# Kernel optimization log

Hardware: AMD Instinct MI355X
Metric: run time of the kernel (lower is better)

## Reference

```python
import jax, jax.numpy as jnp
import numpy as np

B, C, D, Hh, W = 2, 320, 4, 16, 16
N = D * Hh * W          # 1024 nodes
NH = 8                  # num_heads
DH = C // NH            # 40
L = 2                   # num_layers
A, EPD = 16, 64         # da_prior tokens, encode_prior_dim
EDGE_SCALE = 32 ** -0.5 # GraphEdgeFeature dim_head=32
SCALE = DH ** -0.5
EPS = 1e-5


def _ln(x, g, b):
    m = x.mean(-1, keepdims=True)
    v = ((x - m) ** 2).mean(-1, keepdims=True)
    return (x - m) * jax.lax.rsqrt(v + EPS) * g + b


def setup_inputs() -> dict:
    key = jax.random.key(0)
    ks = jax.random.split(key, 16)
    std = 0.02 / np.sqrt(L)
    inp = {
        'x': jax.random.normal(ks[0], (B, C, D, Hh, W), jnp.float32),
        'da_prior': jax.random.normal(ks[1], (B, A, EPD), jnp.float32),
        # GraphEdgeFeature.to_qk (no bias), init std 0.02/sqrt(24)
        'qk_w': jax.random.normal(ks[2], (2 * C, C), jnp.float32) * (0.02 / np.sqrt(24)),
        # fc_prior
        'fcp_w': jax.random.normal(ks[3], (C, EPD), jnp.float32) * 0.02,
        'fcp_b': jnp.zeros((C,), jnp.float32),
        # per-layer (stacked over L)
        'ln1_g': jnp.ones((L, C), jnp.float32),
        'ln1_b': jnp.zeros((L, C), jnp.float32),
        'gln_g': jnp.ones((L, C), jnp.float32),
        'gln_b': jnp.zeros((L, C), jnp.float32),
        'qkv_w': jax.random.normal(ks[4], (L, 3 * C, C), jnp.float32) * std,
        'qkv_b': jnp.zeros((L, 3 * C), jnp.float32),
        'proj_w': jax.random.normal(ks[5], (L, C, C), jnp.float32) * std,
        'proj_b': jnp.zeros((L, C), jnp.float32),
        # expand Conv2d(1, NH, 1): weight [NH], bias [NH]
        'exp_w': jax.random.normal(ks[6], (L, NH), jnp.float32),
        'exp_b': jnp.zeros((L, NH), jnp.float32),
        # reduce Conv2d(NH, 1, 1): weight [NH], bias scalar
        'red_w': jax.random.normal(ks[7], (L, NH), jnp.float32) / np.sqrt(NH),
        'red_b': jnp.zeros((L,), jnp.float32),
    }
    return inp


def _forward(x, da_prior, qk_w, fcp_w, fcp_b, ln1_g, ln1_b, gln_g, gln_b,
             qkv_w, qkv_b, proj_w, proj_b, exp_w, exp_b, red_w, red_b):
    node = x.reshape(B, C, N)                       # [B,C,N]
    # ---- GraphEdgeFeature: full-dim QK attention over nodes ----
    xt = node.transpose(0, 2, 1)                    # [B,N,C]
    qk = xt @ qk_w.T                                # [B,N,2C]
    q_e, k_e = jnp.split(qk, 2, axis=-1)
    edge = jax.nn.softmax(jnp.einsum('bqc,bkc->bqk', q_e, k_e) * EDGE_SCALE, axis=-1)  # [B,N,N]
    # ---- fc_prior ----
    da = da_prior @ fcp_w.T + fcp_b                 # [B,A,C]
    s = da.sum(axis=1)                              # [B,C] (sum over 'a' in einsum bnc,bca->bnc)
    for l in range(L):
        # block norm1 over channel dim
        nt = _ln(node.transpose(0, 2, 1), ln1_g[l], ln1_b[l])   # [B,N,C]
        # torch.einsum('bnn,bnc->bnc') takes the DIAGONAL of edge
        diag = jnp.diagonal(edge, axis1=1, axis2=2)             # [B,N]
        node2 = diag[:, :, None] * nt * s[:, None, :] + nt      # [B,N,C]
        y = _ln(node2, gln_g[l], gln_b[l])
        qkv = (y @ qkv_w[l].T + qkv_b[l]).reshape(B, N, 3, NH, DH)
        qkv = qkv.transpose(2, 0, 3, 1, 4)                      # [3,B,H,N,DH]
        q, k, v = qkv[0], qkv[1], qkv[2]
        attn = jnp.einsum('bhnd,bhmd->bhnm', q, k) * SCALE
        attn = attn + edge[:, None] * exp_w[l][None, :, None, None] + exp_b[l][None, :, None, None]
        a = jax.nn.softmax(attn, axis=-1)                       # [B,H,N,N]
        node_out = jnp.einsum('bhnm,bhmd->bhnd', a, v).transpose(0, 2, 1, 3).reshape(B, N, C)
        edge_new = jnp.einsum('bhnm,h->bnm', a + attn, red_w[l]) + red_b[l]  # [B,N,N]
        ws = jax.nn.softmax(edge_new, axis=-1)
        wsum = (ws * edge_new).sum(-1)                          # [B,N]
        node_out = node_out + wsum[:, :, None]                  # fc=Identity, broadcast
        node_out = node_out @ proj_w[l].T + proj_b[l]
        node = node_out.transpose(0, 2, 1)                      # [B,C,N]
        edge = edge + edge_new
    return node.reshape(B, C, D, Hh, W)


def reference(x, da_prior, qk_w, fcp_w, fcp_b, ln1_g, ln1_b, gln_g, gln_b,
              qkv_w, qkv_b, proj_w, proj_b, exp_w, exp_b, red_w, red_b):
    return _forward(x, da_prior, qk_w, fcp_w, fcp_b, ln1_g, ln1_b, gln_g, gln_b,
                    qkv_w, qkv_b, proj_w, proj_b, exp_w, exp_b, red_w, red_b)
```

## Files before the change

### kernel.cpp

```cpp
#include <hip/hip_runtime.h>
#include <math.h>

#define EDGE_SCALE 0.17677669529663687f
#define ATT_SCALE  0.15811388300841897f
#define INV_ATT    6.324555320336759f
#define LN_EPS 1e-5f

typedef __attribute__((ext_vector_type(8))) short bf8;
typedef __attribute__((ext_vector_type(4))) float f32x4;

__device__ __forceinline__ f32x4 mfma16(bf8 a, bf8 b, f32x4 c) {
  return __builtin_amdgcn_mfma_f32_16x16x32_bf16(a, b, c, 0, 0, 0);
}
__device__ __forceinline__ unsigned short f2bf(float f) {
  union { float f; unsigned u; } v; v.f = f;
  unsigned r = v.u + 0x7FFF + ((v.u >> 16) & 1);
  return (unsigned short)(r >> 16);
}
__device__ __forceinline__ float bf2f(unsigned short h) {
  union { unsigned u; float f; } v; v.u = ((unsigned)h) << 16;
  return v.f;
}
__device__ __forceinline__ float wave_max(float v) {
  #pragma unroll
  for (int o = 32; o > 0; o >>= 1) v = fmaxf(v, __shfl_xor(v, o));
  return v;
}
__device__ __forceinline__ float wave_sum(float v) {
  #pragma unroll
  for (int o = 32; o > 0; o >>= 1) v += __shfl_xor(v, o);
  return v;
}

__global__ __launch_bounds__(256) void k_trans(const float* __restrict__ x,
    float* __restrict__ node, unsigned short* __restrict__ nodebf) {
  __shared__ float tile[32][33];
  const int b = blockIdx.z;
  const int n0 = blockIdx.x * 32, c0 = blockIdx.y * 32;
  const int tx = threadIdx.x & 31, ty = threadIdx.x >> 5;
  #pragma unroll
  for (int k = 0; k < 4; ++k) {
    int c = c0 + ty + 8 * k;
    tile[ty + 8 * k][tx] = x[((size_t)b * 320 + c) * 1024 + n0 + tx];
  }
  __syncthreads();
  #pragma unroll
  for (int k = 0; k < 4; ++k) {
    int n = n0 + ty + 8 * k;
    float v = tile[tx][ty + 8 * k];
    size_t idx = ((size_t)b * 1024 + n) * 320 + c0 + tx;
    node[idx] = v;
    nodebf[idx] = f2bf(v);
  }
}

__global__ __launch_bounds__(320) void k_svec(const float* __restrict__ da,
    const float* __restrict__ fw, const float* __restrict__ fb, float* __restrict__ sv) {
  __shared__ float ds[64];
  const int b = blockIdx.x, t = threadIdx.x;
  if (t < 64) {
    float a = 0.f;
    #pragma unroll
    for (int i = 0; i < 16; ++i) a += da[b * 1024 + i * 64 + t];
    ds[t] = a;
  }
  __syncthreads();
  if (t < 320) {
    float acc = 16.f * fb[t];
    #pragma unroll
    for (int e = 0; e < 64; ++e) acc = fmaf(ds[e], fw[t * 64 + e], acc);
    sv[b * 320 + t] = acc;
  }
}

__global__ void k_wcvt(const float* __restrict__ a, int na,
                       const float* __restrict__ b, int nb,
                       const float* __restrict__ c, int nc,
                       unsigned short* __restrict__ out) {
  int tot = na + nb + nc;
  for (int i = blockIdx.x * blockDim.x + threadIdx.x; i < tot; i += gridDim.x * blockDim.x) {
    float v = (i < na) ? a[i] : ((i < na + nb) ? b[i - na] : c[i - na - nb]);
    out[i] = f2bf(v);
  }
}

__global__ __launch_bounds__(256, 4) void k_mgemm(
    const unsigned short* __restrict__ A, const unsigned short* __restrict__ W,
    const float* __restrict__ bias, void* p0, void* p1, void* p2, int mode) {
  __shared__ float smem[64 * 65];
  const int t = threadIdx.x, w = t >> 6, lane = t & 63;
  const int q16 = lane >> 4, l16 = lane & 15;
  const int rt = blockIdx.x * 64, jt = blockIdx.y * 64;
  f32x4 acc[4];
  #pragma unroll
  for (int i = 0; i < 4; ++i)
    #pragma unroll
    for (int j = 0; j < 4; ++j) acc[i][j] = 0.f;
  const unsigned short* ap = A + (size_t)(rt + 16 * w + l16) * 320 + q16 * 8;
  const unsigned short* wp = W + (size_t)(jt + l16) * 320 + q16 * 8;
  for (int kc = 0; kc < 10; ++kc) {
    bf8 af = *(const bf8*)(ap + kc * 32);
    #pragma unroll
    for (int ct = 0; ct < 4; ++ct) {
      bf8 bf = *(const bf8*)(wp + (size_t)ct * 16 * 320 + kc * 32);
      acc[ct] = mfma16(af, bf, acc[ct]);
    }
  }
  if (mode == 0 || mode == 1) {
    #pragma unroll
    for (int ct = 0; ct < 4; ++ct) {
      int col = jt + ct * 16 + l16;
      float bv = bias ? bias[col] : 0.f;
      #pragma unroll
      for (int r = 0; r < 4; ++r) {
        int row = rt + 16 * w + q16 * 4 + r;
        float v = acc[ct][r] + bv;
        if (mode == 0) {
          ((float*)p0)[(size_t)row * 320 + col] = v;
        } else {
          if (col < 320) ((unsigned short*)p0)[(size_t)row * 320 + col] = f2bf(v);
          else           ((unsigned short*)p1)[(size_t)row * 320 + col - 320] = f2bf(v);
        }
      }
    }
  } else if (mode == 2) {
    const int part = jt / 320;
    if (part < 2) {
      unsigned short* dst = (unsigned short*)(part == 0 ? p0 : p1);
      #pragma unroll
      for (int ct = 0; ct < 4; ++ct) {
        int col = jt + ct * 16 + l16;
        float bv = bias[col];
        int rem = col - part * 320;
        int h = rem / 40, d = rem % 40;
        #pragma unroll
        for (int r = 0; r < 4; ++r) {
          int row = rt + 16 * w + q16 * 4 + r;
          int b = row >> 10, n = row & 1023;
          size_t base = (((size_t)b * 8 + h) * 1024 + n) * 64;
          dst[base + d] = f2bf(acc[ct][r] + bv);
          if (d < 24) dst[base + 40 + d] = 0;
        }
      }
    } else {
      unsigned short* vt_t = (unsigned short*)smem;
      #pragma unroll
      for (int ct = 0; ct < 4; ++ct) {
        int col = jt + ct * 16 + l16;
        float bv = bias[col];
        #pragma unroll
        for (int r = 0; r < 4; ++r)
          vt_t[(ct * 16 + l16) * 72 + 16 * w + q16 * 4 + r] = f2bf(acc[ct][r] + bv);
      }
      __syncthreads();
      const int cl = t >> 2, seg = t & 3;
      int rem = (jt - 640) + cl;
      int h = rem / 40, d = rem % 40;
      int b = rt >> 10, n = (rt & 1023) + seg * 16;
      const float4* lp = (const float4*)&vt_t[cl * 72 + seg * 16];
      float4 a0 = lp[0], a1 = lp[1];
      float4* gp = (float4*)((unsigned short*)p2 +
                             (((size_t)b * 8 + h) * 48 + d) * 1024 + n);
      gp[0] = a0; gp[1] = a1;
    }
  } else {
    #pragma unroll
    for (int ct = 0; ct < 4; ++ct) {
      int col = jt + ct * 16 + l16;
      float bv = bias[col];
      #pragma unroll
      for (int r = 0; r < 4; ++r)
        smem[(16 * w + q16 * 4 + r) * 65 + ct * 16 + l16] = acc[ct][r] + bv;
    }
    __syncthreads();
    const int cl = t >> 2, seg = t & 3;
    int b = rt >> 10, n = (rt & 1023) + seg * 16;
    float* orow = (float*)p0 + ((size_t)b * 320 + jt + cl) * 1024 + n;
    #pragma unroll
    for (int i2 = 0; i2 < 4; ++i2) {
      float4 vv;
      vv.x = smem[(seg * 16 + i2 * 4 + 0) * 65 + cl];
      vv.y = smem[(seg * 16 + i2 * 4 + 1) * 65 + cl];
      vv.z = smem[(seg * 16 + i2 * 4 + 2) * 65 + cl];
      vv.w = smem[(seg * 16 + i2 * 4 + 3) * 65 + cl];
      ((float4*)orow)[i2] = vv;
    }
  }
}

__global__ __launch_bounds__(256, 4) void k_sgemm(
    const unsigned short* __restrict__ qe, const unsigned short* __restrict__ ke,
    float* __restrict__ S) {
  const int t = threadIdx.x, w = t >> 6, lane = t & 63;
  const int q16 = lane >> 4, l16 = lane & 15;
  const int rt = blockIdx.x * 64, jt = blockIdx.y * 64, b = blockIdx.z;
  const unsigned short* A = qe + (size_t)b * 1024 * 320;
  const unsigned short* W = ke + (size_t)b * 1024 * 320;
  f32x4 acc[4];
  #pragma unroll
  for (int i = 0; i < 4; ++i)
    #pragma unroll
    for (int j = 0; j < 4; ++j) acc[i][j] = 0.f;
  const unsigned short* ap = A + (size_t)(rt + 16 * w + l16) * 320 + q16 * 8;
  const unsigned short* wp = W + (size_t)(jt + l16) * 320 + q16 * 8;
  for (int kc = 0; kc < 10; ++kc) {
    bf8 af = *(const bf8*)(ap + kc * 32);
    #pragma unroll
    for (int ct = 0; ct < 4; ++ct) {
      bf8 bf = *(const bf8*)(wp + (size_t)ct * 16 * 320 + kc * 32);
      acc[ct] = mfma16(af, bf, acc[ct]);
    }
  }
  #pragma unroll
  for (int ct = 0; ct < 4; ++ct)
    #pragma unroll
    for (int r = 0; r < 4; ++r)
      S[((size_t)b * 1024 + rt + 16 * w + q16 * 4 + r) * 1024 + jt + ct * 16 + l16] =
          acc[ct][r] * EDGE_SCALE;
}

__global__ __launch_bounds__(256) void k_smax(const float* __restrict__ S,
                                              float* __restrict__ edge) {
  const int w = threadIdx.x >> 6, lane = threadIdx.x & 63;
  const int row = blockIdx.x * 4 + w;
  const float4* sp = (const float4*)(S + (size_t)row * 1024) + lane;
  float4 v[4];
  #pragma unroll
  for (int i = 0; i < 4; ++i) v[i] = sp[i * 64];
  float mx = -3.4e38f;
  #pragma unroll
  for (int i = 0; i < 4; ++i)
    mx = fmaxf(mx, fmaxf(fmaxf(v[i].x, v[i].y), fmaxf(v[i].z, v[i].w)));
  mx = wave_max(mx);
  float s = 0.f;
  #pragma unroll
  for (int i = 0; i < 4; ++i) {
    v[i].x = __expf(v[i].x - mx); v[i].y = __expf(v[i].y - mx);
    v[i].z = __expf(v[i].z - mx); v[i].w = __expf(v[i].w - mx);
    s += v[i].x + v[i].y + v[i].z + v[i].w;
  }
  s = wave_sum(s);
  float inv = 1.f / s;
  float4* ep = (float4*)(edge + (size_t)row * 1024) + lane;
  #pragma unroll
  for (int i = 0; i < 4; ++i)
    ep[i * 64] = make_float4(v[i].x * inv, v[i].y * inv, v[i].z * inv, v[i].w * inv);
}

__global__ __launch_bounds__(256) void k_ln(const float* __restrict__ node,
    const float* __restrict__ edge, const float* __restrict__ sv,
    const float* __restrict__ g1, const float* __restrict__ b1,
    const float* __restrict__ g2, const float* __restrict__ b2,
    unsigned short* __restrict__ y) {
  const int w = threadIdx.x >> 6, lane = threadIdx.x & 63;
  const int row = blockIdx.x * 4 + w;
  const int b = row >> 10, n = row & 1023;
  const float* xr = node + (size_t)row * 320;
  float x[5];
  #pragma unroll
  for (int i = 0; i < 5; ++i) x[i] = xr[lane + 64 * i];
  float s = x[0] + x[1] + x[2] + x[3] + x[4];
  float mean = wave_sum(s) * (1.f / 320.f);
  float v = 0.f;
  #pragma unroll
  for (int i = 0; i < 5; ++i) { float d = x[i] - mean; v += d * d; }
  float rstd = rsqrtf(wave_sum(v) * (1.f / 320.f) + LN_EPS);
  float diag = edge[(size_t)row * 1024 + n];
  float n2[5];
  #pragma unroll
  for (int i = 0; i < 5; ++i) {
    int c = lane + 64 * i;
    float nt = (x[i] - mean) * rstd * g1[c] + b1[c];
    n2[i] = diag * nt * sv[b * 320 + c] + nt;
  }
  s = n2[0] + n2[1] + n2[2] + n2[3] + n2[4];
  float mean2 = wave_sum(s) * (1.f / 320.f);
  v = 0.f;
  #pragma unroll
  for (int i = 0; i < 5; ++i) { float d = n2[i] - mean2; v += d * d; }
  float rstd2 = rsqrtf(wave_sum(v) * (1.f / 320.f) + LN_EPS);
  unsigned short* yr = y + (size_t)row * 320;
  #pragma unroll
  for (int i = 0; i < 5; ++i) {
    int c = lane + 64 * i;
    yr[c] = f2bf((n2[i] - mean2) * rstd2 * g2[c] + b2[c]);
  }
}

__global__ __launch_bounds__(256, 4) void k_score(
    const unsigned short* __restrict__ qbf, const unsigned short* __restrict__ kbf,
    const unsigned short* __restrict__ vtb, const float* __restrict__ edge,
    unsigned short* __restrict__ thbuf, float* __restrict__ att,
    const float* __restrict__ ew, const float* __restrict__ eb,
    const float* __restrict__ rw) {
  __shared__ unsigned short a_lds[4][4][16][20];
  __shared__ unsigned short th_lds[4][16][72];
  __shared__ float ored[4][3][16][17];
  __shared__ float redm[4][16], reds[4][16];
  const int t = threadIdx.x, w = t >> 6, lane = t & 63;
  const int q16 = lane >> 4, l16 = lane & 15;
  const int n0 = blockIdx.x * 16, h = blockIdx.y, b = blockIdx.z;
  const size_t bh = (size_t)b * 8 + h;
  const float ewh = ew[h], ebh = eb[h], rwh = rw[h];
  f32x4 acc[16];
  const float* ep = edge + ((size_t)b * 1024 + n0 + q16 * 4) * 1024 + w * 256 + l16;
  #pragma unroll
  for (int tt = 0; tt < 16; ++tt)
    #pragma unroll
    for (int r = 0; r < 4; ++r)
      acc[tt][r] = fmaf(ep[(size_t)r * 1024 + tt * 16], ewh, ebh) * INV_ATT;
  const unsigned short* qp = qbf + (bh * 1024 + n0 + l16) * 64 + q16 * 8;
  bf8 af0 = *(const bf8*)(qp);
  bf8 af1 = *(const bf8*)(qp + 32);
  const unsigned short* kp = kbf + (bh * 1024 + (size_t)w * 256 + l16) * 64 + q16 * 8;
  #pragma unroll
  for (int tt = 0; tt < 16; ++tt) {
    const unsigned short* kpt = kp + (size_t)tt * 16 * 64;
    bf8 b0 = *(const bf8*)(kpt);
    bf8 b1 = *(const bf8*)(kpt + 32);
    acc[tt] = mfma16(af0, b0, acc[tt]);
    acc[tt] = mfma16(af1, b1, acc[tt]);
  }
  #pragma unroll
  for (int tt = 0; tt < 16; ++tt)
    #pragma unroll
    for (int r = 0; r < 4; ++r) acc[tt][r] *= ATT_SCALE;
  float pm[4] = {-3.4e38f, -3.4e38f, -3.4e38f, -3.4e38f};
  #pragma unroll
  for (int tt = 0; tt < 16; ++tt)
    #pragma unroll
    for (int r = 0; r < 4; ++r) pm[r] = fmaxf(pm[r], acc[tt][r]);
  #pragma unroll
  for (int r = 0; r < 4; ++r)
    #pragma unroll
    for (int o = 1; o <= 8; o <<= 1) pm[r] = fmaxf(pm[r], __shfl_xor(pm[r], o));
  if (l16 == 0) {
    #pragma unroll
    for (int r = 0; r < 4; ++r) redm[w][q16 * 4 + r] = pm[r];
  }
  __syncthreads();
  float m[4], ps[4] = {0.f, 0.f, 0.f, 0.f};
  #pragma unroll
  for (int r = 0; r < 4; ++r)
    m[r] = fmaxf(fmaxf(redm[0][q16 * 4 + r], redm[1][q16 * 4 + r]),
                 fmaxf(redm[2][q16 * 4 + r], redm[3][q16 * 4 + r]));
  #pragma unroll
  for (int tt = 0; tt < 16; ++tt)
    #pragma unroll
    for (int r = 0; r < 4; ++r) ps[r] += __expf(acc[tt][r] - m[r]);
  #pragma unroll
  for (int r = 0; r < 4; ++r)
    #pragma unroll
    for (int o = 1; o <= 8; o <<= 1) ps[r] += __shfl_xor(ps[r], o);
  if (l16 == 0) {
    #pragma unroll
    for (int r = 0; r < 4; ++r) reds[w][q16 * 4 + r] = ps[r];
  }
  __syncthreads();
  float inv[4];
  #pragma unroll
  for (int r = 0; r < 4; ++r)
    inv[r] = 1.f / (reds[0][q16 * 4 + r] + reds[1][q16 * 4 + r] +
                    reds[2][q16 * 4 + r] + reds[3][q16 * 4 + r]);
  f32x4 oacc[3];
  #pragma unroll
  for (int i = 0; i < 3; ++i)
    #pragma unroll
    for (int j = 0; j < 4; ++j) oacc[i][j] = 0.f;
  unsigned short* tbase = thbuf + (bh * 1024 + n0) * 1024 + w * 256;
  const int trow = lane >> 2, tc4 = lane & 3;
  #pragma unroll
  for (int g = 0; g < 4; ++g) {
    #pragma unroll
    for (int ti = 0; ti < 4; ++ti) {
      int tt = g * 4 + ti;
      #pragma unroll
      for (int r = 0; r < 4; ++r) {
        float e = __expf(acc[tt][r] - m[r]);
        float a = e * inv[r];
        a_lds[w][ti][q16 * 4 + r][l16] = f2bf(a);
        th_lds[w][q16 * 4 + r][ti * 16 + l16] = f2bf(rwh * (a + acc[tt][r]));
      }
    }
    #pragma unroll
    for (int kk = 0; kk < 2; ++kk) {
      const unsigned short* ap2 = &a_lds[w][kk * 2 + (q16 >> 1)][l16][(q16 & 1) * 8];
      short4 lo = *(const short4*)(ap2);
      short4 hi = *(const short4*)(ap2 + 4);
      bf8 afv = {lo.x, lo.y, lo.z, lo.w, hi.x, hi.y, hi.z, hi.w};
      int kc = w * 8 + g * 2 + kk;
      const unsigned short* vp = vtb + (bh * 48 + l16) * 1024 + (size_t)kc * 32 + q16 * 8;
      #pragma unroll
      for (int nt = 0; nt < 3; ++nt) {
        bf8 bfv = *(const bf8*)(vp + (size_t)nt * 16 * 1024);
        oacc[nt] = mfma16(afv, bfv, oacc[nt]);
      }
    }
    {
      const float4* lp = (const float4*)&th_lds[w][trow][tc4 * 16];
      float4 v0 = lp[0], v1 = lp[1];
      float4* gp = (float4*)(tbase + (size_t)trow * 1024 + g * 64 + tc4 * 16);
      gp[0] = v0; gp[1] = v1;
    }
  }
  #pragma unroll
  for (int nt = 0; nt < 3; ++nt)
    #pragma unroll
    for (int r = 0; r < 4; ++r) ored[w][nt][q16 * 4 + r][l16] = oacc[nt][r];
  __syncthreads();
  #pragma unroll
  for (int k = 0; k < 3; ++k) {
    int o = k * 256 + t;
    int nt = o >> 8, row = (o >> 4) & 15, col = o & 15;
    int dim = nt * 16 + col;
    float sum = ored[0][nt][row][col] + ored[1][nt][row][col] +
                ored[2][nt][row][col] + ored[3][nt][row][col];
    if (dim < 40)
      att[((size_t)b * 1024 + n0 + row) * 320 + h * 40 + dim] = sum;
  }
}

__global__ __launch_bounds__(256) void k_wsum(
    const unsigned short* __restrict__ thbuf, float* __restrict__ edge,
    const float* __restrict__ att, unsigned short* __restrict__ attbf,
    const float* __restrict__ rb) {
  const int w = threadIdx.x >> 6, lane = threadIdx.x & 63;
  const int row = blockIdx.x * 4 + w;
  const int b = row >> 10, n = row & 1023;
  const float rbv = rb[0];
  float tv[16];
  #pragma unroll
  for (int i = 0; i < 16; ++i) tv[i] = rbv;
  #pragma unroll 1
  for (int h = 0; h < 8; ++h) {
    const unsigned short* tph = thbuf + (((size_t)b * 8 + h) * 1024 + n) * 1024 + lane * 4;
    #pragma unroll
    for (int seg = 0; seg < 4; ++seg) {
      ushort4 u = *(const ushort4*)(tph + seg * 256);
      tv[seg * 4 + 0] += bf2f(u.x);
      tv[seg * 4 + 1] += bf2f(u.y);
      tv[seg * 4 + 2] += bf2f(u.z);
      tv[seg * 4 + 3] += bf2f(u.w);
    }
  }
  float4* erp = (float4*)(edge + ((size_t)b * 1024 + n) * 1024) + lane;
  #pragma unroll
  for (int seg = 0; seg < 4; ++seg) {
    float4 e = erp[seg * 64];
    e.x += tv[seg * 4 + 0]; e.y += tv[seg * 4 + 1];
    e.z += tv[seg * 4 + 2]; e.w += tv[seg * 4 + 3];
    erp[seg * 64] = e;
  }
  float mx = -3.4e38f;
  #pragma unroll
  for (int i = 0; i < 16; ++i) mx = fmaxf(mx, tv[i]);
  mx = wave_max(mx);
  float s = 0.f, num = 0.f;
  #pragma unroll
  for (int i = 0; i < 16; ++i) {
    float e = __expf(tv[i] - mx);
    s += e; num += e * tv[i];
  }
  s = wave_sum(s); num = wave_sum(num);
  const float wsum = num / s;
  const float* ar = att + (size_t)row * 320;
  unsigned short* ao = attbf + (size_t)row * 320;
  #pragma unroll
  for (int i = 0; i < 5; ++i) {
    int c = lane + 64 * i;
    ao[c] = f2bf(ar[c] + wsum);
  }
}

extern "C" void kernel_launch(void* const* d_in, const int* in_sizes, int n_in,
                              void* d_out, int out_size, void* d_ws, size_t ws_size,
                              hipStream_t stream) {
  const float* x      = (const float*)d_in[0];
  const float* da     = (const float*)d_in[1];
  const float* qk_w   = (const float*)d_in[2];
  const float* fcp_w  = (const float*)d_in[3];
  const float* fcp_b  = (const float*)d_in[4];
  const float* ln1_g  = (const float*)d_in[5];
  const float* ln1_b  = (const float*)d_in[6];
  const float* gln_g  = (const float*)d_in[7];
  const float* gln_b  = (const float*)d_in[8];
  const float* qkv_w  = (const float*)d_in[9];
  const float* qkv_b  = (const float*)d_in[10];
  const float* proj_w = (const float*)d_in[11];
  const float* proj_b = (const float*)d_in[12];
  const float* exp_w  = (const float*)d_in[13];
  const float* exp_b  = (const float*)d_in[14];
  const float* red_w  = (const float*)d_in[15];
  const float* red_b  = (const float*)d_in[16];
  float* ws = (float*)d_ws;
  float* node  = ws + 0;
  unsigned short* ybf   = (unsigned short*)(ws + 655360);
  float* attb  = ws + 983040;
  unsigned short* attbf = (unsigned short*)(ws + 1638400);
  float* edge  = ws + 1966080;
  float* svec  = ws + 4063232;
  unsigned short* nodebf = (unsigned short*)(ws + 4063872);
  unsigned short* qe   = (unsigned short*)(ws + 4391552);
  unsigned short* ke   = (unsigned short*)(ws + 4719232);
  unsigned short* qbf  = (unsigned short*)(ws + 5046912);
  unsigned short* kbf  = (unsigned short*)(ws + 5571200);
  unsigned short* vtb  = (unsigned short*)(ws + 6095488);
  unsigned short* wbf  = (unsigned short*)(ws + 6488704);
  unsigned short* thbuf= (unsigned short*)(ws + 7000704);
  float* sbuf = ws + 15389312;
  float* out = (float*)d_out;
  unsigned short* qk_wb   = wbf;
  unsigned short* qkv_wb  = wbf + 204800;
  unsigned short* proj_wb = wbf + 819200;

  hipLaunchKernelGGL(k_trans, dim3(32, 10, 2), dim3(256), 0, stream, x, node, nodebf);
  hipLaunchKernelGGL(k_svec, dim3(2), dim3(320), 0, stream, da, fcp_w, fcp_b, svec);
  hipLaunchKernelGGL(k_wcvt, dim3(512), dim3(256), 0, stream,
                     qk_w, 204800, qkv_w, 614400, proj_w, 204800, wbf);
  hipLaunchKernelGGL(k_mgemm, dim3(32, 10), dim3(256), 0, stream,
                     nodebf, qk_wb, (const float*)nullptr, qe, ke, (void*)nullptr, 1);
  hipLaunchKernelGGL(k_sgemm, dim3(16, 16, 2), dim3(256), 0, stream, qe, ke, sbuf);
  hipLaunchKernelGGL(k_smax, dim3(512), dim3(256), 0, stream, sbuf, edge);
  for (int l = 0; l < 2; ++l) {
    hipLaunchKernelGGL(k_ln, dim3(512), dim3(256), 0, stream, node, edge, svec,
                       ln1_g + l * 320, ln1_b + l * 320, gln_g + l * 320, gln_b + l * 320, ybf);
    hipLaunchKernelGGL(k_mgemm, dim3(32, 15), dim3(256), 0, stream,
                       ybf, qkv_wb + (size_t)l * 307200, qkv_b + l * 960, qbf, kbf, vtb, 2);
    hipLaunchKernelGGL(k_score, dim3(64, 8, 2), dim3(256), 0, stream,
                       qbf, kbf, vtb, edge, thbuf, attb,
                       exp_w + l * 8, exp_b + l * 8, red_w + l * 8);
    hipLaunchKernelGGL(k_wsum, dim3(512), dim3(256), 0, stream,
                       thbuf, edge, attb, attbf, red_b + l);
    if (l == 0)
      hipLaunchKernelGGL(k_mgemm, dim3(32, 5), dim3(256), 0, stream,
                         attbf, proj_wb, proj_b, node, (void*)nullptr, (void*)nullptr, 0);
    else
      hipLaunchKernelGGL(k_mgemm, dim3(32, 5), dim3(256), 0, stream,
                         attbf, proj_wb + 102400, proj_b + 320, out,
                         (void*)nullptr, (void*)nullptr, 3);
  }
}
```

Before: 297.1 us.

## Recompute attention scores for head-reduced edge update instead of storing per-head tensor

The score kernel no longer writes the per-head bf16 edge contribution tensor [B,H,N,N]. It stores only the softmax row max and inverse sum per row. A new kernel recomputes QK scores per head with MFMA, rebuilds the softmax probabilities from those stats, reduces across heads, updates edge, and writes a single bf16 [B,N,N] buffer that a lighter wsum kernel consumes. This trades roughly 32MB of intermediate HBM traffic per layer for a second QK matmul pass and one extra kernel launch.

```diff
diff --git a/kernel.cpp b/kernel.cpp
--- a/kernel.cpp
+++ b/kernel.cpp
@@ -290,18 +290,16 @@
 __global__ __launch_bounds__(256, 4) void k_score(
     const unsigned short* __restrict__ qbf, const unsigned short* __restrict__ kbf,
     const unsigned short* __restrict__ vtb, const float* __restrict__ edge,
-    unsigned short* __restrict__ thbuf, float* __restrict__ att,
-    const float* __restrict__ ew, const float* __restrict__ eb,
-    const float* __restrict__ rw) {
+    float* __restrict__ att, float2* __restrict__ minv,
+    const float* __restrict__ ew, const float* __restrict__ eb) {
   __shared__ unsigned short a_lds[4][4][16][20];
-  __shared__ unsigned short th_lds[4][16][72];
   __shared__ float ored[4][3][16][17];
   __shared__ float redm[4][16], reds[4][16];
   const int t = threadIdx.x, w = t >> 6, lane = t & 63;
   const int q16 = lane >> 4, l16 = lane & 15;
   const int n0 = blockIdx.x * 16, h = blockIdx.y, b = blockIdx.z;
   const size_t bh = (size_t)b * 8 + h;
-  const float ewh = ew[h], ebh = eb[h], rwh = rw[h];
+  const float ewh = ew[h], ebh = eb[h];
   f32x4 acc[16];
   const float* ep = edge + ((size_t)b * 1024 + n0 + q16 * 4) * 1024 + w * 256 + l16;
   #pragma unroll
@@ -362,13 +360,16 @@
   for (int r = 0; r < 4; ++r)
     inv[r] = 1.f / (reds[0][q16 * 4 + r] + reds[1][q16 * 4 + r] +
                     reds[2][q16 * 4 + r] + reds[3][q16 * 4 + r]);
+  if (w == 0 && l16 == 0) {
+    #pragma unroll
+    for (int r = 0; r < 4; ++r)
+      minv[bh * 1024 + n0 + q16 * 4 + r] = make_float2(m[r], inv[r]);
+  }
   f32x4 oacc[3];
   #pragma unroll
   for (int i = 0; i < 3; ++i)
     #pragma unroll
     for (int j = 0; j < 4; ++j) oacc[i][j] = 0.f;
-  unsigned short* tbase = thbuf + (bh * 1024 + n0) * 1024 + w * 256;
-  const int trow = lane >> 2, tc4 = lane & 3;
   #pragma unroll
   for (int g = 0; g < 4; ++g) {
     #pragma unroll
@@ -377,9 +378,7 @@
       #pragma unroll
       for (int r = 0; r < 4; ++r) {
         float e = __expf(acc[tt][r] - m[r]);
-        float a = e * inv[r];
-        a_lds[w][ti][q16 * 4 + r][l16] = f2bf(a);
-        th_lds[w][q16 * 4 + r][ti * 16 + l16] = f2bf(rwh * (a + acc[tt][r]));
+        a_lds[w][ti][q16 * 4 + r][l16] = f2bf(e * inv[r]);
       }
     }
     #pragma unroll
@@ -395,12 +394,6 @@
         bf8 bfv = *(const bf8*)(vp + (size_t)nt * 16 * 1024);
         oacc[nt] = mfma16(afv, bfv, oacc[nt]);
       }
-    }
-    {
-      const float4* lp = (const float4*)&th_lds[w][trow][tc4 * 16];
-      float4 v0 = lp[0], v1 = lp[1];
-      float4* gp = (float4*)(tbase + (size_t)trow * 1024 + g * 64 + tc4 * 16);
-      gp[0] = v0; gp[1] = v1;
     }
   }
   #pragma unroll
@@ -420,36 +413,82 @@
   }
 }
 
-__global__ __launch_bounds__(256) void k_wsum(
-    const unsigned short* __restrict__ thbuf, float* __restrict__ edge,
-    const float* __restrict__ att, unsigned short* __restrict__ attbf,
-    const float* __restrict__ rb) {
+__global__ __launch_bounds__(256, 4) void k_tred(
+    const unsigned short* __restrict__ qbf, const unsigned short* __restrict__ kbf,
+    float* __restrict__ edge, const float2* __restrict__ minv,
+    unsigned short* __restrict__ tbf,
+    const float* __restrict__ ew, const float* __restrict__ eb,
+    const float* __restrict__ rw, const float* __restrict__ rb) {
+  const int t = threadIdx.x, w = t >> 6, lane = t & 63;
+  const int q16 = lane >> 4, l16 = lane & 15;
+  const int bid = blockIdx.x;
+  const int b = bid >> 9, rest = bid & 511;
+  const int n0 = (rest >> 3) * 16;
+  const int m0 = (rest & 7) * 128 + w * 32;
+  const float rbv = rb[0];
+  float ev[2][4], tacc[2][4];
+  const float* ep = edge + ((size_t)b * 1024 + n0 + q16 * 4) * 1024 + m0 + l16;
+  #pragma unroll
+  for (int tt = 0; tt < 2; ++tt)
+    #pragma unroll
+    for (int r = 0; r < 4; ++r) {
+      ev[tt][r] = ep[(size_t)r * 1024 + tt * 16];
+      tacc[tt][r] = rbv;
+    }
+  #pragma unroll 1
+  for (int h = 0; h < 8; ++h) {
+    const size_t bh = (size_t)b * 8 + h;
+    const float ewh = ew[h], ebh = eb[h], rwh = rw[h];
+    const unsigned short* qp = qbf + (bh * 1024 + n0 + l16) * 64 + q16 * 8;
+    bf8 af0 = *(const bf8*)(qp);
+    bf8 af1 = *(const bf8*)(qp + 32);
+    const unsigned short* kp = kbf + (bh * 1024 + m0 + l16) * 64 + q16 * 8;
+    float2 mv[4];
+    #pragma unroll
+    for (int r = 0; r < 4; ++r) mv[r] = minv[bh * 1024 + n0 + q16 * 4 + r];
+    #pragma unroll
+    for (int tt = 0; tt < 2; ++tt) {
+      const unsigned short* kpt = kp + (size_t)tt * 16 * 64;
+      bf8 b0 = *(const bf8*)(kpt);
+      bf8 b1 = *(const bf8*)(kpt + 32);
+      f32x4 acc;
+      #pragma unroll
+      for (int r = 0; r < 4; ++r) acc[r] = fmaf(ev[tt][r], ewh, ebh) * INV_ATT;
+      acc = mfma16(af0, b0, acc);
+      acc = mfma16(af1, b1, acc);
+      #pragma unroll
+      for (int r = 0; r < 4; ++r) {
+        float s = acc[r] * ATT_SCALE;
+        float a = __expf(s - mv[r].x) * mv[r].y;
+        tacc[tt][r] += rwh * (a + s);
+      }
+    }
+  }
+  #pragma unroll
+  for (int tt = 0; tt < 2; ++tt)
+    #pragma unroll
+    for (int r = 0; r < 4; ++r) {
+      size_t idx = ((size_t)b * 1024 + n0 + q16 * 4 + r) * 1024 + m0 + tt * 16 + l16;
+      float tv = tacc[tt][r];
+      edge[idx] = ev[tt][r] + tv;
+      tbf[idx] = f2bf(tv);
+    }
+}
+
+__global__ __launch_bounds__(256) void k_ws(
+    const unsigned short* __restrict__ tbf, const float* __restrict__ att,
+    unsigned short* __restrict__ attbf) {
   const int w = threadIdx.x >> 6, lane = threadIdx.x & 63;
   const int row = blockIdx.x * 4 + w;
-  const int b = row >> 10, n = row & 1023;
-  const float rbv = rb[0];
+  const unsigned short* tp = tbf + (size_t)row * 1024 + lane * 4;
   float tv[16];
   #pragma unroll
-  for (int i = 0; i < 16; ++i) tv[i] = rbv;
-  #pragma unroll 1
-  for (int h = 0; h < 8; ++h) {
-    const unsigned short* tph = thbuf + (((size_t)b * 8 + h) * 1024 + n) * 1024 + lane * 4;
-    #pragma unroll
-    for (int seg = 0; seg < 4; ++seg) {
-      ushort4 u = *(const ushort4*)(tph + seg * 256);
-      tv[seg * 4 + 0] += bf2f(u.x);
-      tv[seg * 4 + 1] += bf2f(u.y);
-      tv[seg * 4 + 2] += bf2f(u.z);
-      tv[seg * 4 + 3] += bf2f(u.w);
-    }
-  }
-  float4* erp = (float4*)(edge + ((size_t)b * 1024 + n) * 1024) + lane;
-  #pragma unroll
   for (int seg = 0; seg < 4; ++seg) {
-    float4 e = erp[seg * 64];
-    e.x += tv[seg * 4 + 0]; e.y += tv[seg * 4 + 1];
-    e.z += tv[seg * 4 + 2]; e.w += tv[seg * 4 + 3];
-    erp[seg * 64] = e;
+    ushort4 u = *(const ushort4*)(tp + seg * 256);
+    tv[seg * 4 + 0] = bf2f(u.x);
+    tv[seg * 4 + 1] = bf2f(u.y);
+    tv[seg * 4 + 2] = bf2f(u.z);
+    tv[seg * 4 + 3] = bf2f(u.w);
   }
   float mx = -3.4e38f;
   #pragma unroll
@@ -506,7 +545,8 @@
   unsigned short* kbf  = (unsigned short*)(ws + 5571200);
   unsigned short* vtb  = (unsigned short*)(ws + 6095488);
   unsigned short* wbf  = (unsigned short*)(ws + 6488704);
-  unsigned short* thbuf= (unsigned short*)(ws + 7000704);
+  unsigned short* tbf  = (unsigned short*)(ws + 7000704);
+  float2* minv = (float2*)(ws + 7000704 + 1048576);
   float* sbuf = ws + 15389312;
   float* out = (float*)d_out;
   unsigned short* qk_wb   = wbf;
@@ -527,10 +567,12 @@
     hipLaunchKernelGGL(k_mgemm, dim3(32, 15), dim3(256), 0, stream,
                        ybf, qkv_wb + (size_t)l * 307200, qkv_b + l * 960, qbf, kbf, vtb, 2);
     hipLaunchKernelGGL(k_score, dim3(64, 8, 2), dim3(256), 0, stream,
-                       qbf, kbf, vtb, edge, thbuf, attb,
-                       exp_w + l * 8, exp_b + l * 8, red_w + l * 8);
-    hipLaunchKernelGGL(k_wsum, dim3(512), dim3(256), 0, stream,
-                       thbuf, edge, attb, attbf, red_b + l);
+                       qbf, kbf, vtb, edge, attb, minv,
+                       exp_w + l * 8, exp_b + l * 8);
+    hipLaunchKernelGGL(k_tred, dim3(1024), dim3(256), 0, stream,
+                       qbf, kbf, edge, minv, tbf,
+                       exp_w + l * 8, exp_b + l * 8, red_w + l * 8, red_b + l);
+    hipLaunchKernelGGL(k_ws, dim3(512), dim3(256), 0, stream, tbf, attb, attbf);
     if (l == 0)
       hipLaunchKernelGGL(k_mgemm, dim3(32, 5), dim3(256), 0, stream,
                          attbf, proj_wb, proj_b, node, (void*)nullptr, (void*)nullptr, 0);
```

Result: slower. 309.7 us (+4.2%).
